# Performance work log

Measured on AMD Instinct MI355X. Metric: run time of the kernel, lower is better.

Reference implementation:

```python
import jax, jax.numpy as jnp
import numpy as np

IN_FEATS, N_HIDDEN, N_CLASSES = 128, 256, 32
N0, N1, B = 614400, 40960, 4096
F0, F1 = 15, 10
BN_EPS = 1e-5


def setup_inputs() -> dict:
    key = jax.random.key(0)
    ks = jax.random.split(key, 20)
    s = 0.02
    inp = {
        "x": jax.random.uniform(ks[0], (N0, IN_FEATS), jnp.float32) * 10.0,
        "nbr0": jax.random.randint(ks[1], (N1, F0), 0, N0, jnp.int32),
        "nbr1": jax.random.randint(ks[2], (B, F1), 0, N1, jnp.int32),
        # layer0: SAGEConv(128->256, 'pool')
        "W_pool": jax.random.normal(ks[3], (IN_FEATS, IN_FEATS), jnp.float32) * s,
        "b_pool": jnp.zeros((IN_FEATS,), jnp.float32),
        "W_self0": jax.random.normal(ks[4], (N_HIDDEN, IN_FEATS), jnp.float32) * s,
        "W_neigh0": jax.random.normal(ks[5], (N_HIDDEN, IN_FEATS), jnp.float32) * s,
        "b0": jnp.zeros((N_HIDDEN,), jnp.float32),
        # BatchNorm1d(n_hidden)
        "gamma0": jnp.ones((N_HIDDEN,), jnp.float32),
        "beta0": jnp.zeros((N_HIDDEN,), jnp.float32),
        # layer1: SAGEConv(256->32, 'lstm'); torch LSTM gate order i,f,g,o
        "W_ih": jax.random.normal(ks[6], (4 * N_HIDDEN, N_HIDDEN), jnp.float32) * s,
        "W_hh": jax.random.normal(ks[7], (4 * N_HIDDEN, N_HIDDEN), jnp.float32) * s,
        "b_ih": jnp.zeros((4 * N_HIDDEN,), jnp.float32),
        "b_hh": jnp.zeros((4 * N_HIDDEN,), jnp.float32),
        "W_self1": jax.random.normal(ks[8], (N_CLASSES, N_HIDDEN), jnp.float32) * s,
        "W_neigh1": jax.random.normal(ks[9], (N_CLASSES, N_HIDDEN), jnp.float32) * s,
        "b1": jnp.zeros((N_CLASSES,), jnp.float32),
    }
    return inp


def _lstm_agg(seq, W_ih, W_hh, b_ih, b_hh):
    # seq: [B, K, H]; run LSTM over K neighbor steps, return final hidden [B, H]
    Bsz, _, H = seq.shape
    xs = jnp.swapaxes(seq, 0, 1)  # [K, B, H]

    def step(carry, x_t):
        h_t, c_t = carry
        g = x_t @ W_ih.T + b_ih + h_t @ W_hh.T + b_hh  # [B, 4H]
        i, f, gg, o = jnp.split(g, 4, axis=-1)
        c = jax.nn.sigmoid(f) * c_t + jax.nn.sigmoid(i) * jnp.tanh(gg)
        h = jax.nn.sigmoid(o) * jnp.tanh(c)
        return (h, c), None

    init = (jnp.zeros((Bsz, H), seq.dtype), jnp.zeros((Bsz, H), seq.dtype))
    (hT, _), _ = jax.lax.scan(step, init, xs)
    return hT


def reference(x, nbr0, nbr1, W_pool, b_pool, W_self0, W_neigh0, b0,
              gamma0, beta0, W_ih, W_hh, b_ih, b_hh, W_self1, W_neigh1, b1):
    n1 = nbr0.shape[0]
    b = nbr1.shape[0]
    h = jnp.log(x + 1.0)  # [N0, in_feats]

    # --- layer 0: SAGEConv 'pool' ---
    hp = jax.nn.relu(h @ W_pool.T + b_pool)           # [N0, in_feats]
    h_neigh = jnp.max(hp[nbr0], axis=1)               # [N1, in_feats]
    h0 = h[:n1] @ W_self0.T + h_neigh @ W_neigh0.T + b0  # [N1, n_hidden]

    # BN (training stats) + relu (dropout p=0)
    mu = jnp.mean(h0, axis=0)
    var = jnp.var(h0, axis=0)
    h0 = (h0 - mu) * jax.lax.rsqrt(var + BN_EPS) * gamma0 + beta0
    h0 = jax.nn.relu(h0)

    # --- layer 1: SAGEConv 'lstm' ---
    seq = h0[nbr1]                                    # [B, F1, n_hidden]
    h_neigh1 = _lstm_agg(seq, W_ih, W_hh, b_ih, b_hh)  # [B, n_hidden]
    out = h0[:b] @ W_self1.T + h_neigh1 @ W_neigh1.T + b1  # [B, n_classes]
    return out
```

## Files before the change

kernel.cpp:

```cpp
#include <hip/hip_runtime.h>

#define N0v 614400
#define N1v 40960
#define BATCHv 4096

typedef __attribute__((ext_vector_type(8))) short short8;
typedef __attribute__((ext_vector_type(4))) float floatx4;

static __device__ __forceinline__ float flog1p(float v) { return __logf(v + 1.0f); }
static __device__ __forceinline__ float sigf(float v) { return 1.0f / (1.0f + __expf(-v)); }
static __device__ __forceinline__ float tanhfast(float v) {
    return 1.0f - 2.0f / (__expf(2.0f * v) + 1.0f);
}
static __device__ __forceinline__ unsigned short f2bf(float f) {
    union { float f; unsigned u; } v; v.f = f;
    unsigned r = v.u + 0x7FFFu + ((v.u >> 16) & 1u);
    return (unsigned short)(r >> 16);
}
static __device__ __forceinline__ float bf2f(unsigned short u) {
    return __uint_as_float(((unsigned)u) << 16);
}

__global__ __launch_bounds__(256) void cvt_weights_kernel(
    const float* __restrict__ Wp, const float* __restrict__ Ws0,
    const float* __restrict__ Wn0, const float* __restrict__ Wih,
    const float* __restrict__ Whh, const float* __restrict__ bih,
    const float* __restrict__ bhh,
    unsigned short* __restrict__ Wpb, unsigned short* __restrict__ Ws0b,
    unsigned short* __restrict__ Wn0b, unsigned short* __restrict__ Wihb,
    unsigned short* __restrict__ Whhb, float* __restrict__ bsum)
{
    const int g = blockIdx.x * 256 + threadIdx.x;
    if (g < 16384)            Wpb[g] = f2bf(Wp[g]);
    else if (g < 49152)       Ws0b[g - 16384] = f2bf(Ws0[g - 16384]);
    else if (g < 81920)       Wn0b[g - 49152] = f2bf(Wn0[g - 49152]);
    else if (g < 344064)      Wihb[g - 81920] = f2bf(Wih[g - 81920]);
    else if (g < 606208)      Whhb[g - 344064] = f2bf(Whh[g - 344064]);
    else if (g < 607232) { const int i = g - 606208; bsum[i] = bih[i] + bhh[i]; }
}

__global__ __launch_bounds__(256) void pool_max_kernel(
    const float* __restrict__ x, const int* __restrict__ nbr0,
    const unsigned short* __restrict__ Wpb, const float* __restrict__ bp,
    unsigned short* __restrict__ hnb)
{
    __shared__ unsigned short smem[64 * 72 + 128 * 72];
    __shared__ unsigned red[512];
    __shared__ int nodes[64];
    unsigned short* aT = smem;
    unsigned short* wT = smem + 64 * 72;

    const int tid = threadIdx.x;
    const size_t base = (size_t)blockIdx.x * 60;
    if (tid < 64) nodes[tid] = (tid < 60) ? nbr0[base + tid] : 0;
    for (int i = tid; i < 512; i += 256) red[i] = 0u;

    const int lane = tid & 63, wv = tid >> 6;
    const int ml = lane & 15, q = lane >> 4, qk = q * 8;

    floatx4 acc[8];
#pragma unroll
    for (int ct = 0; ct < 8; ++ct) acc[ct] = (floatx4){0.f, 0.f, 0.f, 0.f};

    for (int kc = 0; kc < 2; ++kc) {
        __syncthreads();
        for (int i = tid; i < 512; i += 256) {
            const int row = i >> 3, seg = i & 7;
            short8 o = {0, 0, 0, 0, 0, 0, 0, 0};
            if (row < 60) {
                const float* s = x + (size_t)nodes[row] * 128 + kc * 64 + seg * 8;
                const float4 f0 = *(const float4*)s;
                const float4 f1 = *(const float4*)(s + 4);
                o[0] = (short)f2bf(flog1p(f0.x)); o[1] = (short)f2bf(flog1p(f0.y));
                o[2] = (short)f2bf(flog1p(f0.z)); o[3] = (short)f2bf(flog1p(f0.w));
                o[4] = (short)f2bf(flog1p(f1.x)); o[5] = (short)f2bf(flog1p(f1.y));
                o[6] = (short)f2bf(flog1p(f1.z)); o[7] = (short)f2bf(flog1p(f1.w));
            }
            *(short8*)&aT[row * 72 + seg * 8] = o;
        }
        for (int i = tid; i < 1024; i += 256) {
            const int row = i >> 3, seg = i & 7;
            *(short8*)&wT[row * 72 + seg * 8] =
                *(const short8*)&Wpb[(size_t)row * 128 + kc * 64 + seg * 8];
        }
        __syncthreads();
#pragma unroll
        for (int k0 = 0; k0 < 64; k0 += 32) {
            const short8 a = *(const short8*)&aT[(wv * 16 + ml) * 72 + k0 + qk];
#pragma unroll
            for (int ct = 0; ct < 8; ++ct) {
                const short8 b = *(const short8*)&wT[(ct * 16 + ml) * 72 + k0 + qk];
                acc[ct] = __builtin_amdgcn_mfma_f32_16x16x32_bf16(a, b, acc[ct], 0, 0, 0);
            }
        }
    }
    __syncthreads();
#pragma unroll
    for (int ct = 0; ct < 8; ++ct) {
        const int col = ct * 16 + ml;
        const float bb = bp[col];
#pragma unroll
        for (int r = 0; r < 4; ++r) {
            const int row = wv * 16 + q * 4 + r;
            if (row < 60) {
                const float v = fmaxf(acc[ct][r] + bb, 0.0f);
                atomicMax(&red[(row / 15) * 128 + col], __float_as_uint(v));
            }
        }
    }
    __syncthreads();
    for (int i = tid; i < 512; i += 256)
        hnb[(size_t)blockIdx.x * 512 + i] = f2bf(__uint_as_float(red[i]));
}

__global__ __launch_bounds__(256) void h0_kernel(
    const float* __restrict__ x, const unsigned short* __restrict__ hnb,
    const unsigned short* __restrict__ Ws0b, const unsigned short* __restrict__ Wn0b,
    const float* __restrict__ b0, unsigned short* __restrict__ h0bf,
    float* __restrict__ bn_sum, float* __restrict__ bn_sq)
{
    __shared__ unsigned short smem[64 * 72 + 128 * 72];
    unsigned short* aT = smem;
    unsigned short* wT = smem + 64 * 72;

    const int tid = threadIdx.x;
    const int m0 = blockIdx.x * 64, c0 = blockIdx.y * 128;
    const int lane = tid & 63, wv = tid >> 6;
    const int ml = lane & 15, q = lane >> 4, qk = q * 8;

    floatx4 acc[8];
#pragma unroll
    for (int ct = 0; ct < 8; ++ct) acc[ct] = (floatx4){0.f, 0.f, 0.f, 0.f};

    for (int kc = 0; kc < 4; ++kc) {
        __syncthreads();
        for (int i = tid; i < 512; i += 256) {
            const int row = i >> 3, seg = i & 7;
            const int k = kc * 64 + seg * 8;
            if (kc < 2) {
                const float* s = x + (size_t)(m0 + row) * 128 + k;
                const float4 f0 = *(const float4*)s;
                const float4 f1 = *(const float4*)(s + 4);
                short8 o;
                o[0] = (short)f2bf(flog1p(f0.x)); o[1] = (short)f2bf(flog1p(f0.y));
                o[2] = (short)f2bf(flog1p(f0.z)); o[3] = (short)f2bf(flog1p(f0.w));
                o[4] = (short)f2bf(flog1p(f1.x)); o[5] = (short)f2bf(flog1p(f1.y));
                o[6] = (short)f2bf(flog1p(f1.z)); o[7] = (short)f2bf(flog1p(f1.w));
                *(short8*)&aT[row * 72 + seg * 8] = o;
            } else {
                *(short8*)&aT[row * 72 + seg * 8] =
                    *(const short8*)&hnb[(size_t)(m0 + row) * 128 + (k - 128)];
            }
        }
        for (int i = tid; i < 1024; i += 256) {
            const int row = i >> 3, seg = i & 7;
            const int k = kc * 64 + seg * 8;
            const size_t cg = (size_t)(c0 + row);
            *(short8*)&wT[row * 72 + seg * 8] = (kc < 2)
                ? *(const short8*)&Ws0b[cg * 128 + k]
                : *(const short8*)&Wn0b[cg * 128 + (k - 128)];
        }
        __syncthreads();
#pragma unroll
        for (int k0 = 0; k0 < 64; k0 += 32) {
            const short8 a = *(const short8*)&aT[(wv * 16 + ml) * 72 + k0 + qk];
#pragma unroll
            for (int ct = 0; ct < 8; ++ct) {
                const short8 b = *(const short8*)&wT[(ct * 16 + ml) * 72 + k0 + qk];
                acc[ct] = __builtin_amdgcn_mfma_f32_16x16x32_bf16(a, b, acc[ct], 0, 0, 0);
            }
        }
    }
    __syncthreads();
    float* scr = (float*)smem;
#pragma unroll
    for (int ct = 0; ct < 8; ++ct) {
        const int col = ct * 16 + ml, cg = c0 + col;
        const float bb = b0[cg];
        float s = 0.f, sq = 0.f;
#pragma unroll
        for (int r = 0; r < 4; ++r) {
            const int row = wv * 16 + q * 4 + r;
            const float v = acc[ct][r] + bb;
            h0bf[(size_t)(m0 + row) * 256 + cg] = f2bf(v);
            s += v; sq += v * v;
        }
        scr[(wv * 4 + q) * 128 + col] = s;
        scr[2048 + (wv * 4 + q) * 128 + col] = sq;
    }
    __syncthreads();
    if (tid < 128) {
        float s = 0.f, sq = 0.f;
#pragma unroll
        for (int j = 0; j < 16; ++j) {
            s += scr[j * 128 + tid];
            sq += scr[2048 + j * 128 + tid];
        }
        atomicAdd(&bn_sum[c0 + tid], s);
        atomicAdd(&bn_sq[c0 + tid], sq);
    }
}

__global__ void bn_stats_kernel(const float* __restrict__ bn_sum, const float* __restrict__ bn_sq,
                                const float* __restrict__ gamma, const float* __restrict__ beta,
                                float* __restrict__ scale, float* __restrict__ shift)
{
    const int c = threadIdx.x;
    const float inv_n = 1.0f / (float)N1v;
    const float mu = bn_sum[c] * inv_n;
    const float var = bn_sq[c] * inv_n - mu * mu;
    const float rs = rsqrtf(var + 1e-5f);
    const float sc = rs * gamma[c];
    scale[c] = sc;
    shift[c] = beta[c] - mu * sc;
}

__global__ __launch_bounds__(256) void bn_apply_kernel(
    const unsigned short* __restrict__ h0bf, const float* __restrict__ scale,
    const float* __restrict__ shift, unsigned short* __restrict__ h0nbf)
{
    const int gid = blockIdx.x * 256 + threadIdx.x;
    const int c0 = (gid * 8) & 255;
    const short8 v = *(const short8*)&h0bf[(size_t)gid * 8];
    short8 o;
#pragma unroll
    for (int j = 0; j < 8; ++j) {
        const float f = bf2f((unsigned short)v[j]);
        o[j] = (short)f2bf(fmaxf(fmaf(f, scale[c0 + j], shift[c0 + j]), 0.0f));
    }
    *(short8*)&h0nbf[(size_t)gid * 8] = o;
}

__global__ __launch_bounds__(256) void lstm_step_kernel(
    const unsigned short* __restrict__ h0nbf, const int* __restrict__ nbr1,
    const unsigned short* __restrict__ hbprev, const unsigned short* __restrict__ Wihb,
    const unsigned short* __restrict__ Whhb, const float* __restrict__ bsum,
    float* __restrict__ cst, unsigned short* __restrict__ hb, int t)
{
    __shared__ unsigned short smem[64 * 72 + 128 * 72];
    __shared__ int nodes[64];
    unsigned short* aT = smem;
    unsigned short* wT = smem + 64 * 72;

    const int tid = threadIdx.x;
    const int m0 = blockIdx.x * 64, c0h = blockIdx.y * 32;
    const int lane = tid & 63, wv = tid >> 6;
    const int ml = lane & 15, q = lane >> 4, qk = q * 8;

    if (tid < 64) nodes[tid] = nbr1[(size_t)(m0 + tid) * 10 + t];

    floatx4 acc[8];
#pragma unroll
    for (int ct = 0; ct < 8; ++ct) acc[ct] = (floatx4){0.f, 0.f, 0.f, 0.f};

    const int kcN = (t == 0) ? 4 : 8;
    for (int kc = 0; kc < kcN; ++kc) {
        __syncthreads();
        for (int i = tid; i < 512; i += 256) {
            const int row = i >> 3, seg = i & 7;
            const int k = kc * 64 + seg * 8;
            *(short8*)&aT[row * 72 + seg * 8] = (kc < 4)
                ? *(const short8*)&h0nbf[(size_t)nodes[row] * 256 + k]
                : *(const short8*)&hbprev[(size_t)(m0 + row) * 256 + (k - 256)];
        }
        for (int i = tid; i < 1024; i += 256) {
            const int row = i >> 3, seg = i & 7;
            const int k = kc * 64 + seg * 8;
            const size_t wr = (size_t)((row >> 5) * 256 + c0h + (row & 31));
            *(short8*)&wT[row * 72 + seg * 8] = (kc < 4)
                ? *(const short8*)&Wihb[wr * 256 + k]
                : *(const short8*)&Whhb[wr * 256 + (k - 256)];
        }
        __syncthreads();
#pragma unroll
        for (int k0 = 0; k0 < 64; k0 += 32) {
            const short8 a = *(const short8*)&aT[(wv * 16 + ml) * 72 + k0 + qk];
#pragma unroll
            for (int ct = 0; ct < 8; ++ct) {
                const short8 b = *(const short8*)&wT[(ct * 16 + ml) * 72 + k0 + qk];
                acc[ct] = __builtin_amdgcn_mfma_f32_16x16x32_bf16(a, b, acc[ct], 0, 0, 0);
            }
        }
    }
#pragma unroll
    for (int hg = 0; hg < 2; ++hg) {
        const int hcol = hg * 16 + ml;
        const float bi = bsum[c0h + hcol];
        const float bf_ = bsum[256 + c0h + hcol];
        const float bg = bsum[512 + c0h + hcol];
        const float bo = bsum[768 + c0h + hcol];
#pragma unroll
        for (int r = 0; r < 4; ++r) {
            const int row = wv * 16 + q * 4 + r;
            const size_t idx = (size_t)(m0 + row) * 256 + c0h + hcol;
            const float gi = acc[hg][r] + bi;
            const float gf = acc[2 + hg][r] + bf_;
            const float gg = acc[4 + hg][r] + bg;
            const float go = acc[6 + hg][r] + bo;
            float c = sigf(gi) * tanhfast(gg);
            if (t > 0) c += sigf(gf) * cst[idx];
            cst[idx] = c;
            hb[idx] = f2bf(sigf(go) * tanhfast(c));
        }
    }
}

__global__ __launch_bounds__(256) void out_kernel(
    const unsigned short* __restrict__ h0nbf, const unsigned short* __restrict__ hTb,
    const float* __restrict__ Ws1, const float* __restrict__ Wn1,
    const float* __restrict__ b1, float* __restrict__ out)
{
    const int gid = blockIdx.x * 256 + threadIdx.x;
    const int row = gid >> 5, c = gid & 31;
    const unsigned short* a0 = h0nbf + (size_t)row * 256;
    const unsigned short* a1 = hTb + (size_t)row * 256;
    const float* w0 = Ws1 + (size_t)c * 256;
    const float* w1 = Wn1 + (size_t)c * 256;
    float s = b1[c];
#pragma unroll 4
    for (int k8 = 0; k8 < 32; ++k8) {
        const short8 av = *(const short8*)&a0[k8 * 8];
        const short8 bv = *(const short8*)&a1[k8 * 8];
        const float4 wa0 = *(const float4*)&w0[k8 * 8];
        const float4 wa1 = *(const float4*)&w0[k8 * 8 + 4];
        const float4 wb0 = *(const float4*)&w1[k8 * 8];
        const float4 wb1 = *(const float4*)&w1[k8 * 8 + 4];
        s += bf2f((unsigned short)av[0]) * wa0.x + bf2f((unsigned short)av[1]) * wa0.y;
        s += bf2f((unsigned short)av[2]) * wa0.z + bf2f((unsigned short)av[3]) * wa0.w;
        s += bf2f((unsigned short)av[4]) * wa1.x + bf2f((unsigned short)av[5]) * wa1.y;
        s += bf2f((unsigned short)av[6]) * wa1.z + bf2f((unsigned short)av[7]) * wa1.w;
        s += bf2f((unsigned short)bv[0]) * wb0.x + bf2f((unsigned short)bv[1]) * wb0.y;
        s += bf2f((unsigned short)bv[2]) * wb0.z + bf2f((unsigned short)bv[3]) * wb0.w;
        s += bf2f((unsigned short)bv[4]) * wb1.x + bf2f((unsigned short)bv[5]) * wb1.y;
        s += bf2f((unsigned short)bv[6]) * wb1.z + bf2f((unsigned short)bv[7]) * wb1.w;
    }
    out[gid] = s;
}

extern "C" void kernel_launch(void* const* d_in, const int* in_sizes, int n_in,
                              void* d_out, int out_size, void* d_ws, size_t ws_size,
                              hipStream_t stream)
{
    const float* x        = (const float*)d_in[0];
    const int*   nbr0     = (const int*)d_in[1];
    const int*   nbr1     = (const int*)d_in[2];
    const float* W_pool   = (const float*)d_in[3];
    const float* b_pool   = (const float*)d_in[4];
    const float* W_self0  = (const float*)d_in[5];
    const float* W_neigh0 = (const float*)d_in[6];
    const float* b0       = (const float*)d_in[7];
    const float* gamma0   = (const float*)d_in[8];
    const float* beta0    = (const float*)d_in[9];
    const float* W_ih     = (const float*)d_in[10];
    const float* W_hh     = (const float*)d_in[11];
    const float* b_ih     = (const float*)d_in[12];
    const float* b_hh     = (const float*)d_in[13];
    const float* W_self1  = (const float*)d_in[14];
    const float* W_neigh1 = (const float*)d_in[15];
    const float* b1       = (const float*)d_in[16];
    float* out = (float*)d_out;

    char* ws = (char*)d_ws;
    unsigned short* h0bf  = (unsigned short*)(ws);
    unsigned short* hnb   = (unsigned short*)(ws + 20971520);
    unsigned short* h0nbf = (unsigned short*)(ws + 31457280);
    float*          cst   = (float*)(ws + 52428800);
    unsigned short* hb0   = (unsigned short*)(ws + 56623104);
    unsigned short* hb1   = (unsigned short*)(ws + 58720256);
    unsigned short* Wpb   = (unsigned short*)(ws + 60817408);
    unsigned short* Ws0b  = (unsigned short*)(ws + 60850176);
    unsigned short* Wn0b  = (unsigned short*)(ws + 60915712);
    unsigned short* Wihb  = (unsigned short*)(ws + 60981248);
    unsigned short* Whhb  = (unsigned short*)(ws + 61505536);
    float*          bsum  = (float*)(ws + 62029824);
    float*          bn_sum   = (float*)(ws + 62033920);
    float*          bn_sq    = (float*)(ws + 62034944);
    float*          bn_scale = (float*)(ws + 62035968);
    float*          bn_shift = (float*)(ws + 62036992);

    hipMemsetAsync(bn_sum, 0, 2048, stream);

    cvt_weights_kernel<<<2372, 256, 0, stream>>>(W_pool, W_self0, W_neigh0, W_ih, W_hh,
                                                 b_ih, b_hh, Wpb, Ws0b, Wn0b, Wihb, Whhb, bsum);
    pool_max_kernel<<<N1v / 4, 256, 0, stream>>>(x, nbr0, Wpb, b_pool, hnb);
    h0_kernel<<<dim3(N1v / 64, 2), 256, 0, stream>>>(x, hnb, Ws0b, Wn0b, b0,
                                                     h0bf, bn_sum, bn_sq);
    bn_stats_kernel<<<1, 256, 0, stream>>>(bn_sum, bn_sq, gamma0, beta0, bn_scale, bn_shift);
    bn_apply_kernel<<<(N1v * 256 / 8) / 256, 256, 0, stream>>>(h0bf, bn_scale, bn_shift, h0nbf);

    for (int t = 0; t < 10; ++t) {
        const unsigned short* hp = (t & 1) ? hb1 : hb0;
        unsigned short*       hn = (t & 1) ? hb0 : hb1;
        lstm_step_kernel<<<dim3(BATCHv / 64, 8), 256, 0, stream>>>(
            h0nbf, nbr1, hp, Wihb, Whhb, bsum, cst, hn, t);
    }
    out_kernel<<<(BATCHv * 32) / 256, 256, 0, stream>>>(h0nbf, hb0, W_self1, W_neigh1, b1, out);
}
```

Measured before the change: 777.1 us.

## Fuse BN apply, LSTM recurrence and output projection into one persistent kernel

Replaces the BN-apply kernel, the ten per-step LSTM launches and the output kernel with one kernel. Each 512-thread block owns 32 batch rows and keeps h in LDS and c in registers across all steps. BN plus ReLU is applied on the fly to the gathered neighbor rows, and weight fragments are streamed straight from global/L2 with register double-buffering instead of LDS staging. This removes launch overhead, the BN-apply pass and the h/c round trips through global memory. In exchange only 128 blocks are launched, each re-reading the full 1 MB bf16 weight set every step, which may leave the GPU underoccupied.

Result: slower. 885.3 us (+13.9%).

```diff
diff --git a/kernel.cpp b/kernel.cpp
--- a/kernel.cpp
+++ b/kernel.cpp
@@ -215,126 +215,159 @@
     shift[c] = beta[c] - mu * sc;
 }
 
-__global__ __launch_bounds__(256) void bn_apply_kernel(
-    const unsigned short* __restrict__ h0bf, const float* __restrict__ scale,
-    const float* __restrict__ shift, unsigned short* __restrict__ h0nbf)
-{
-    const int gid = blockIdx.x * 256 + threadIdx.x;
-    const int c0 = (gid * 8) & 255;
-    const short8 v = *(const short8*)&h0bf[(size_t)gid * 8];
-    short8 o;
-#pragma unroll
-    for (int j = 0; j < 8; ++j) {
-        const float f = bf2f((unsigned short)v[j]);
-        o[j] = (short)f2bf(fmaxf(fmaf(f, scale[c0 + j], shift[c0 + j]), 0.0f));
-    }
-    *(short8*)&h0nbf[(size_t)gid * 8] = o;
-}
-
-__global__ __launch_bounds__(256) void lstm_step_kernel(
-    const unsigned short* __restrict__ h0nbf, const int* __restrict__ nbr1,
-    const unsigned short* __restrict__ hbprev, const unsigned short* __restrict__ Wihb,
-    const unsigned short* __restrict__ Whhb, const float* __restrict__ bsum,
-    float* __restrict__ cst, unsigned short* __restrict__ hb, int t)
-{
-    __shared__ unsigned short smem[64 * 72 + 128 * 72];
-    __shared__ int nodes[64];
-    unsigned short* aT = smem;
-    unsigned short* wT = smem + 64 * 72;
+__global__ __launch_bounds__(512, 2) void lstm_persist_kernel(
+    const unsigned short* __restrict__ h0bf, const int* __restrict__ nbr1,
+    const unsigned short* __restrict__ Wihb, const unsigned short* __restrict__ Whhb,
+    const float* __restrict__ bsum, const float* __restrict__ bn_scale,
+    const float* __restrict__ bn_shift, const float* __restrict__ Ws1,
+    const float* __restrict__ Wn1, const float* __restrict__ b1,
+    float* __restrict__ out)
+{
+    __shared__ unsigned short aT[32 * 520];
+    __shared__ float sc[256], sh[256];
+    __shared__ int nodes[32];
 
     const int tid = threadIdx.x;
-    const int m0 = blockIdx.x * 64, c0h = blockIdx.y * 32;
+    const int m0 = blockIdx.x * 32;
     const int lane = tid & 63, wv = tid >> 6;
     const int ml = lane & 15, q = lane >> 4, qk = q * 8;
 
-    if (tid < 64) nodes[tid] = nbr1[(size_t)(m0 + tid) * 10 + t];
-
-    floatx4 acc[8];
-#pragma unroll
-    for (int ct = 0; ct < 8; ++ct) acc[ct] = (floatx4){0.f, 0.f, 0.f, 0.f};
-
-    const int kcN = (t == 0) ? 4 : 8;
-    for (int kc = 0; kc < kcN; ++kc) {
-        __syncthreads();
-        for (int i = tid; i < 512; i += 256) {
-            const int row = i >> 3, seg = i & 7;
-            const int k = kc * 64 + seg * 8;
-            *(short8*)&aT[row * 72 + seg * 8] = (kc < 4)
-                ? *(const short8*)&h0nbf[(size_t)nodes[row] * 256 + k]
-                : *(const short8*)&hbprev[(size_t)(m0 + row) * 256 + (k - 256)];
-        }
-        for (int i = tid; i < 1024; i += 256) {
-            const int row = i >> 3, seg = i & 7;
-            const int k = kc * 64 + seg * 8;
-            const size_t wr = (size_t)((row >> 5) * 256 + c0h + (row & 31));
-            *(short8*)&wT[row * 72 + seg * 8] = (kc < 4)
-                ? *(const short8*)&Wihb[wr * 256 + k]
-                : *(const short8*)&Whhb[wr * 256 + (k - 256)];
-        }
-        __syncthreads();
-#pragma unroll
-        for (int k0 = 0; k0 < 64; k0 += 32) {
-            const short8 a = *(const short8*)&aT[(wv * 16 + ml) * 72 + k0 + qk];
+    if (tid < 256) { sc[tid] = bn_scale[tid]; sh[tid] = bn_shift[tid]; }
+
+    int wroff[8];
+#pragma unroll
+    for (int ct = 0; ct < 8; ++ct)
+        wroff[ct] = ((ct >> 1) * 256 + wv * 32 + (ct & 1) * 16 + ml) * 256;
+
+    float bias[4][2];
+#pragma unroll
+    for (int g = 0; g < 4; ++g)
+#pragma unroll
+        for (int hg = 0; hg < 2; ++hg)
+            bias[g][hg] = bsum[g * 256 + wv * 32 + hg * 16 + ml];
+
+    float cs[2][2][4];
+#pragma unroll
+    for (int rt = 0; rt < 2; ++rt)
+#pragma unroll
+        for (int hg = 0; hg < 2; ++hg)
+#pragma unroll
+            for (int r = 0; r < 4; ++r) cs[rt][hg][r] = 0.f;
+
+    for (int t = 0; t < 10; ++t) {
+        if (tid < 32) nodes[tid] = nbr1[(size_t)(m0 + tid) * 10 + t];
+        __syncthreads();
+        for (int i = tid; i < 1024; i += 512) {
+            const int row = i >> 5, seg = i & 31;
+            const short8 v = *(const short8*)&h0bf[(size_t)nodes[row] * 256 + seg * 8];
+            short8 o;
+#pragma unroll
+            for (int j = 0; j < 8; ++j) {
+                const float f = fmaxf(fmaf(bf2f((unsigned short)v[j]),
+                                           sc[seg * 8 + j], sh[seg * 8 + j]), 0.0f);
+                o[j] = (short)f2bf(f);
+            }
+            *(short8*)&aT[row * 520 + seg * 8] = o;
+        }
+        __syncthreads();
+
+        floatx4 acc[2][8];
+#pragma unroll
+        for (int rt = 0; rt < 2; ++rt)
+#pragma unroll
+            for (int ct = 0; ct < 8; ++ct) acc[rt][ct] = (floatx4){0.f, 0.f, 0.f, 0.f};
+
+        const int ksN = (t == 0) ? 8 : 16;
+        short8 bcur[8], bnxt[8];
+#pragma unroll
+        for (int ct = 0; ct < 8; ++ct)
+            bcur[ct] = *(const short8*)&Wihb[wroff[ct] + qk];
+        for (int ks = 0; ks < ksN; ++ks) {
+            const int ksn = ks + 1;
+            if (ksn < ksN) {
+                const unsigned short* wb = (ksn < 8) ? Wihb : Whhb;
+                const int koff = (ksn & 7) * 32 + qk;
+#pragma unroll
+                for (int ct = 0; ct < 8; ++ct)
+                    bnxt[ct] = *(const short8*)&wb[wroff[ct] + koff];
+            }
+            const short8 a0 = *(const short8*)&aT[ml * 520 + ks * 32 + qk];
+            const short8 a1 = *(const short8*)&aT[(16 + ml) * 520 + ks * 32 + qk];
 #pragma unroll
             for (int ct = 0; ct < 8; ++ct) {
-                const short8 b = *(const short8*)&wT[(ct * 16 + ml) * 72 + k0 + qk];
-                acc[ct] = __builtin_amdgcn_mfma_f32_16x16x32_bf16(a, b, acc[ct], 0, 0, 0);
-            }
-        }
-    }
-#pragma unroll
-    for (int hg = 0; hg < 2; ++hg) {
-        const int hcol = hg * 16 + ml;
-        const float bi = bsum[c0h + hcol];
-        const float bf_ = bsum[256 + c0h + hcol];
-        const float bg = bsum[512 + c0h + hcol];
-        const float bo = bsum[768 + c0h + hcol];
-#pragma unroll
-        for (int r = 0; r < 4; ++r) {
-            const int row = wv * 16 + q * 4 + r;
-            const size_t idx = (size_t)(m0 + row) * 256 + c0h + hcol;
-            const float gi = acc[hg][r] + bi;
-            const float gf = acc[2 + hg][r] + bf_;
-            const float gg = acc[4 + hg][r] + bg;
-            const float go = acc[6 + hg][r] + bo;
-            float c = sigf(gi) * tanhfast(gg);
-            if (t > 0) c += sigf(gf) * cst[idx];
-            cst[idx] = c;
-            hb[idx] = f2bf(sigf(go) * tanhfast(c));
-        }
-    }
-}
-
-__global__ __launch_bounds__(256) void out_kernel(
-    const unsigned short* __restrict__ h0nbf, const unsigned short* __restrict__ hTb,
-    const float* __restrict__ Ws1, const float* __restrict__ Wn1,
-    const float* __restrict__ b1, float* __restrict__ out)
-{
-    const int gid = blockIdx.x * 256 + threadIdx.x;
-    const int row = gid >> 5, c = gid & 31;
-    const unsigned short* a0 = h0nbf + (size_t)row * 256;
-    const unsigned short* a1 = hTb + (size_t)row * 256;
-    const float* w0 = Ws1 + (size_t)c * 256;
-    const float* w1 = Wn1 + (size_t)c * 256;
-    float s = b1[c];
+                acc[0][ct] = __builtin_amdgcn_mfma_f32_16x16x32_bf16(a0, bcur[ct], acc[0][ct], 0, 0, 0);
+                acc[1][ct] = __builtin_amdgcn_mfma_f32_16x16x32_bf16(a1, bcur[ct], acc[1][ct], 0, 0, 0);
+            }
+#pragma unroll
+            for (int ct = 0; ct < 8; ++ct) bcur[ct] = bnxt[ct];
+        }
+
+        unsigned short hv[2][2][4];
+#pragma unroll
+        for (int rt = 0; rt < 2; ++rt)
+#pragma unroll
+            for (int hg = 0; hg < 2; ++hg)
+#pragma unroll
+                for (int r = 0; r < 4; ++r) {
+                    const float gi = acc[rt][0 + hg][r] + bias[0][hg];
+                    const float gf = acc[rt][2 + hg][r] + bias[1][hg];
+                    const float gg = acc[rt][4 + hg][r] + bias[2][hg];
+                    const float go = acc[rt][6 + hg][r] + bias[3][hg];
+                    float c = sigf(gi) * tanhfast(gg);
+                    if (t > 0) c += sigf(gf) * cs[rt][hg][r];
+                    cs[rt][hg][r] = c;
+                    hv[rt][hg][r] = f2bf(sigf(go) * tanhfast(c));
+                }
+        __syncthreads();
+#pragma unroll
+        for (int rt = 0; rt < 2; ++rt)
+#pragma unroll
+            for (int hg = 0; hg < 2; ++hg)
+#pragma unroll
+                for (int r = 0; r < 4; ++r)
+                    aT[(rt * 16 + q * 4 + r) * 520 + 256 + wv * 32 + hg * 16 + ml] =
+                        hv[rt][hg][r];
+    }
+
+    for (int i = tid; i < 1024; i += 512) {
+        const int row = i >> 5, seg = i & 31;
+        const short8 v = *(const short8*)&h0bf[(size_t)(m0 + row) * 256 + seg * 8];
+        short8 o;
+#pragma unroll
+        for (int j = 0; j < 8; ++j) {
+            const float f = fmaxf(fmaf(bf2f((unsigned short)v[j]),
+                                       sc[seg * 8 + j], sh[seg * 8 + j]), 0.0f);
+            o[j] = (short)f2bf(f);
+        }
+        *(short8*)&aT[row * 520 + seg * 8] = o;
+    }
+    __syncthreads();
+
+    for (int e = tid; e < 1024; e += 512) {
+        const int row = e >> 5, cls = e & 31;
+        const float* w0 = Ws1 + (size_t)cls * 256;
+        const float* w1 = Wn1 + (size_t)cls * 256;
+        const unsigned short* ar = &aT[row * 520];
+        float s = b1[cls];
 #pragma unroll 4
-    for (int k8 = 0; k8 < 32; ++k8) {
-        const short8 av = *(const short8*)&a0[k8 * 8];
-        const short8 bv = *(const short8*)&a1[k8 * 8];
-        const float4 wa0 = *(const float4*)&w0[k8 * 8];
-        const float4 wa1 = *(const float4*)&w0[k8 * 8 + 4];
-        const float4 wb0 = *(const float4*)&w1[k8 * 8];
-        const float4 wb1 = *(const float4*)&w1[k8 * 8 + 4];
-        s += bf2f((unsigned short)av[0]) * wa0.x + bf2f((unsigned short)av[1]) * wa0.y;
-        s += bf2f((unsigned short)av[2]) * wa0.z + bf2f((unsigned short)av[3]) * wa0.w;
-        s += bf2f((unsigned short)av[4]) * wa1.x + bf2f((unsigned short)av[5]) * wa1.y;
-        s += bf2f((unsigned short)av[6]) * wa1.z + bf2f((unsigned short)av[7]) * wa1.w;
-        s += bf2f((unsigned short)bv[0]) * wb0.x + bf2f((unsigned short)bv[1]) * wb0.y;
-        s += bf2f((unsigned short)bv[2]) * wb0.z + bf2f((unsigned short)bv[3]) * wb0.w;
-        s += bf2f((unsigned short)bv[4]) * wb1.x + bf2f((unsigned short)bv[5]) * wb1.y;
-        s += bf2f((unsigned short)bv[6]) * wb1.z + bf2f((unsigned short)bv[7]) * wb1.w;
-    }
-    out[gid] = s;
+        for (int k8 = 0; k8 < 32; ++k8) {
+            const short8 av = *(const short8*)&ar[k8 * 8];
+            const short8 bv = *(const short8*)&ar[256 + k8 * 8];
+            const float4 wa0 = *(const float4*)&w0[k8 * 8];
+            const float4 wa1 = *(const float4*)&w0[k8 * 8 + 4];
+            const float4 wb0 = *(const float4*)&w1[k8 * 8];
+            const float4 wb1 = *(const float4*)&w1[k8 * 8 + 4];
+            s += bf2f((unsigned short)av[0]) * wa0.x + bf2f((unsigned short)av[1]) * wa0.y;
+            s += bf2f((unsigned short)av[2]) * wa0.z + bf2f((unsigned short)av[3]) * wa0.w;
+            s += bf2f((unsigned short)av[4]) * wa1.x + bf2f((unsigned short)av[5]) * wa1.y;
+            s += bf2f((unsigned short)av[6]) * wa1.z + bf2f((unsigned short)av[7]) * wa1.w;
+            s += bf2f((unsigned short)bv[0]) * wb0.x + bf2f((unsigned short)bv[1]) * wb0.y;
+            s += bf2f((unsigned short)bv[2]) * wb0.z + bf2f((unsigned short)bv[3]) * wb0.w;
+            s += bf2f((unsigned short)bv[4]) * wb1.x + bf2f((unsigned short)bv[5]) * wb1.y;
+            s += bf2f((unsigned short)bv[6]) * wb1.z + bf2f((unsigned short)bv[7]) * wb1.w;
+        }
+        out[(size_t)(m0 + row) * 32 + cls] = s;
+    }
 }
 
 extern "C" void kernel_launch(void* const* d_in, const int* in_sizes, int n_in,
@@ -363,10 +396,6 @@
     char* ws = (char*)d_ws;
     unsigned short* h0bf  = (unsigned short*)(ws);
     unsigned short* hnb   = (unsigned short*)(ws + 20971520);
-    unsigned short* h0nbf = (unsigned short*)(ws + 31457280);
-    float*          cst   = (float*)(ws + 52428800);
-    unsigned short* hb0   = (unsigned short*)(ws + 56623104);
-    unsigned short* hb1   = (unsigned short*)(ws + 58720256);
     unsigned short* Wpb   = (unsigned short*)(ws + 60817408);
     unsigned short* Ws0b  = (unsigned short*)(ws + 60850176);
     unsigned short* Wn0b  = (unsigned short*)(ws + 60915712);
@@ -386,13 +415,6 @@
     h0_kernel<<<dim3(N1v / 64, 2), 256, 0, stream>>>(x, hnb, Ws0b, Wn0b, b0,
                                                      h0bf, bn_sum, bn_sq);
     bn_stats_kernel<<<1, 256, 0, stream>>>(bn_sum, bn_sq, gamma0, beta0, bn_scale, bn_shift);
-    bn_apply_kernel<<<(N1v * 256 / 8) / 256, 256, 0, stream>>>(h0bf, bn_scale, bn_shift, h0nbf);
-
-    for (int t = 0; t < 10; ++t) {
-        const unsigned short* hp = (t & 1) ? hb1 : hb0;
-        unsigned short*       hn = (t & 1) ? hb0 : hb1;
-        lstm_step_kernel<<<dim3(BATCHv / 64, 8), 256, 0, stream>>>(
-            h0nbf, nbr1, hp, Wihb, Whhb, bsum, cst, hn, t);
-    }
-    out_kernel<<<(BATCHv * 32) / 256, 256, 0, stream>>>(h0nbf, hb0, W_self1, W_neigh1, b1, out);
-}
+    lstm_persist_kernel<<<BATCHv / 32, 512, 0, stream>>>(
+        h0bf, nbr1, Wihb, Whhb, bsum, bn_scale, bn_shift, W_self1, W_neigh1, b1, out);
+}
```

## Fuse BatchNorm apply into LSTM gather and output; double pool tile rows

Applied to the files above, without the earlier changes.

Removes the separate bn_apply pass over the full 40960x256 hidden matrix. The scale, shift and ReLU are now applied on the fly where rows are gathered, in the LSTM step kernel and in a reworked output kernel that stages its rows in shared memory. The pool-max kernel now handles 120 neighbor rows per block with two row tiles per wave, so each block loads the pool weights once for twice the work. The trade-off is that the BN transform is recomputed on every gather over 10 LSTM steps, and the pool kernel uses more LDS and registers, which may lower occupancy.

Result: slower. 797.4 us (+2.6%).

```diff
diff --git a/kernel.cpp b/kernel.cpp
--- a/kernel.cpp
+++ b/kernel.cpp
@@ -44,30 +44,32 @@
     const unsigned short* __restrict__ Wpb, const float* __restrict__ bp,
     unsigned short* __restrict__ hnb)
 {
-    __shared__ unsigned short smem[64 * 72 + 128 * 72];
-    __shared__ unsigned red[512];
-    __shared__ int nodes[64];
+    __shared__ unsigned short smem[128 * 72 + 128 * 72];
+    __shared__ unsigned red[1024];
+    __shared__ int nodes[128];
     unsigned short* aT = smem;
-    unsigned short* wT = smem + 64 * 72;
+    unsigned short* wT = smem + 128 * 72;
 
     const int tid = threadIdx.x;
-    const size_t base = (size_t)blockIdx.x * 60;
-    if (tid < 64) nodes[tid] = (tid < 60) ? nbr0[base + tid] : 0;
-    for (int i = tid; i < 512; i += 256) red[i] = 0u;
+    const size_t base = (size_t)blockIdx.x * 120;
+    if (tid < 128) nodes[tid] = (tid < 120) ? nbr0[base + tid] : 0;
+    for (int i = tid; i < 1024; i += 256) red[i] = 0u;
 
     const int lane = tid & 63, wv = tid >> 6;
     const int ml = lane & 15, q = lane >> 4, qk = q * 8;
 
-    floatx4 acc[8];
-#pragma unroll
-    for (int ct = 0; ct < 8; ++ct) acc[ct] = (floatx4){0.f, 0.f, 0.f, 0.f};
+    floatx4 acc[2][8];
+#pragma unroll
+    for (int rt = 0; rt < 2; ++rt)
+#pragma unroll
+        for (int ct = 0; ct < 8; ++ct) acc[rt][ct] = (floatx4){0.f, 0.f, 0.f, 0.f};
 
     for (int kc = 0; kc < 2; ++kc) {
         __syncthreads();
-        for (int i = tid; i < 512; i += 256) {
+        for (int i = tid; i < 1024; i += 256) {
             const int row = i >> 3, seg = i & 7;
             short8 o = {0, 0, 0, 0, 0, 0, 0, 0};
-            if (row < 60) {
+            if (row < 120) {
                 const float* s = x + (size_t)nodes[row] * 128 + kc * 64 + seg * 8;
                 const float4 f0 = *(const float4*)s;
                 const float4 f1 = *(const float4*)(s + 4);
@@ -86,31 +88,36 @@
         __syncthreads();
 #pragma unroll
         for (int k0 = 0; k0 < 64; k0 += 32) {
-            const short8 a = *(const short8*)&aT[(wv * 16 + ml) * 72 + k0 + qk];
-#pragma unroll
-            for (int ct = 0; ct < 8; ++ct) {
-                const short8 b = *(const short8*)&wT[(ct * 16 + ml) * 72 + k0 + qk];
-                acc[ct] = __builtin_amdgcn_mfma_f32_16x16x32_bf16(a, b, acc[ct], 0, 0, 0);
-            }
-        }
-    }
-    __syncthreads();
-#pragma unroll
-    for (int ct = 0; ct < 8; ++ct) {
-        const int col = ct * 16 + ml;
-        const float bb = bp[col];
-#pragma unroll
-        for (int r = 0; r < 4; ++r) {
-            const int row = wv * 16 + q * 4 + r;
-            if (row < 60) {
-                const float v = fmaxf(acc[ct][r] + bb, 0.0f);
-                atomicMax(&red[(row / 15) * 128 + col], __float_as_uint(v));
-            }
-        }
-    }
-    __syncthreads();
-    for (int i = tid; i < 512; i += 256)
-        hnb[(size_t)blockIdx.x * 512 + i] = f2bf(__uint_as_float(red[i]));
+#pragma unroll
+            for (int rt = 0; rt < 2; ++rt) {
+                const short8 a = *(const short8*)&aT[((rt * 4 + wv) * 16 + ml) * 72 + k0 + qk];
+#pragma unroll
+                for (int ct = 0; ct < 8; ++ct) {
+                    const short8 b = *(const short8*)&wT[(ct * 16 + ml) * 72 + k0 + qk];
+                    acc[rt][ct] = __builtin_amdgcn_mfma_f32_16x16x32_bf16(a, b, acc[rt][ct], 0, 0, 0);
+                }
+            }
+        }
+    }
+    __syncthreads();
+#pragma unroll
+    for (int rt = 0; rt < 2; ++rt)
+#pragma unroll
+        for (int ct = 0; ct < 8; ++ct) {
+            const int col = ct * 16 + ml;
+            const float bb = bp[col];
+#pragma unroll
+            for (int r = 0; r < 4; ++r) {
+                const int row = (rt * 4 + wv) * 16 + q * 4 + r;
+                if (row < 120) {
+                    const float v = fmaxf(acc[rt][ct][r] + bb, 0.0f);
+                    atomicMax(&red[(row / 15) * 128 + col], __float_as_uint(v));
+                }
+            }
+        }
+    __syncthreads();
+    for (int i = tid; i < 1024; i += 256)
+        hnb[(size_t)blockIdx.x * 1024 + i] = f2bf(__uint_as_float(red[i]));
 }
 
 __global__ __launch_bounds__(256) void h0_kernel(
@@ -215,29 +222,15 @@
     shift[c] = beta[c] - mu * sc;
 }
 
-__global__ __launch_bounds__(256) void bn_apply_kernel(
-    const unsigned short* __restrict__ h0bf, const float* __restrict__ scale,
-    const float* __restrict__ shift, unsigned short* __restrict__ h0nbf)
-{
-    const int gid = blockIdx.x * 256 + threadIdx.x;
-    const int c0 = (gid * 8) & 255;
-    const short8 v = *(const short8*)&h0bf[(size_t)gid * 8];
-    short8 o;
-#pragma unroll
-    for (int j = 0; j < 8; ++j) {
-        const float f = bf2f((unsigned short)v[j]);
-        o[j] = (short)f2bf(fmaxf(fmaf(f, scale[c0 + j], shift[c0 + j]), 0.0f));
-    }
-    *(short8*)&h0nbf[(size_t)gid * 8] = o;
-}
-
 __global__ __launch_bounds__(256) void lstm_step_kernel(
-    const unsigned short* __restrict__ h0nbf, const int* __restrict__ nbr1,
+    const unsigned short* __restrict__ h0bf, const int* __restrict__ nbr1,
     const unsigned short* __restrict__ hbprev, const unsigned short* __restrict__ Wihb,
     const unsigned short* __restrict__ Whhb, const float* __restrict__ bsum,
+    const float* __restrict__ bn_scale, const float* __restrict__ bn_shift,
     float* __restrict__ cst, unsigned short* __restrict__ hb, int t)
 {
     __shared__ unsigned short smem[64 * 72 + 128 * 72];
+    __shared__ float scl[256], shl[256];
     __shared__ int nodes[64];
     unsigned short* aT = smem;
     unsigned short* wT = smem + 64 * 72;
@@ -248,6 +241,8 @@
     const int ml = lane & 15, q = lane >> 4, qk = q * 8;
 
     if (tid < 64) nodes[tid] = nbr1[(size_t)(m0 + tid) * 10 + t];
+    scl[tid] = bn_scale[tid];
+    shl[tid] = bn_shift[tid];
 
     floatx4 acc[8];
 #pragma unroll
@@ -259,9 +254,20 @@
         for (int i = tid; i < 512; i += 256) {
             const int row = i >> 3, seg = i & 7;
             const int k = kc * 64 + seg * 8;
-            *(short8*)&aT[row * 72 + seg * 8] = (kc < 4)
-                ? *(const short8*)&h0nbf[(size_t)nodes[row] * 256 + k]
-                : *(const short8*)&hbprev[(size_t)(m0 + row) * 256 + (k - 256)];
+            if (kc < 4) {
+                const short8 v = *(const short8*)&h0bf[(size_t)nodes[row] * 256 + k];
+                short8 o;
+#pragma unroll
+                for (int j = 0; j < 8; ++j) {
+                    const float f = fmaxf(fmaf(bf2f((unsigned short)v[j]),
+                                               scl[k + j], shl[k + j]), 0.0f);
+                    o[j] = (short)f2bf(f);
+                }
+                *(short8*)&aT[row * 72 + seg * 8] = o;
+            } else {
+                *(short8*)&aT[row * 72 + seg * 8] =
+                    *(const short8*)&hbprev[(size_t)(m0 + row) * 256 + (k - 256)];
+            }
         }
         for (int i = tid; i < 1024; i += 256) {
             const int row = i >> 3, seg = i & 7;
@@ -306,17 +312,47 @@
 }
 
 __global__ __launch_bounds__(256) void out_kernel(
-    const unsigned short* __restrict__ h0nbf, const unsigned short* __restrict__ hTb,
+    const unsigned short* __restrict__ h0bf, const unsigned short* __restrict__ hTb,
+    const float* __restrict__ bn_scale, const float* __restrict__ bn_shift,
     const float* __restrict__ Ws1, const float* __restrict__ Wn1,
     const float* __restrict__ b1, float* __restrict__ out)
 {
-    const int gid = blockIdx.x * 256 + threadIdx.x;
-    const int row = gid >> 5, c = gid & 31;
-    const unsigned short* a0 = h0nbf + (size_t)row * 256;
-    const unsigned short* a1 = hTb + (size_t)row * 256;
-    const float* w0 = Ws1 + (size_t)c * 256;
-    const float* w1 = Wn1 + (size_t)c * 256;
-    float s = b1[c];
+    __shared__ unsigned short aS[8 * 256];
+    __shared__ unsigned short hS[8 * 256];
+    __shared__ float scl[256], shl[256];
+
+    const int tid = threadIdx.x;
+    const int m0 = blockIdx.x * 8;
+    scl[tid] = bn_scale[tid];
+    shl[tid] = bn_shift[tid];
+    __syncthreads();
+
+    for (int i = tid; i < 512; i += 256) {
+        const int sel = i >> 8, idx = i & 255;
+        const int row = idx >> 5, seg = idx & 31;
+        if (sel == 0) {
+            const short8 v = *(const short8*)&h0bf[(size_t)(m0 + row) * 256 + seg * 8];
+            short8 o;
+#pragma unroll
+            for (int j = 0; j < 8; ++j) {
+                const float f = fmaxf(fmaf(bf2f((unsigned short)v[j]),
+                                           scl[seg * 8 + j], shl[seg * 8 + j]), 0.0f);
+                o[j] = (short)f2bf(f);
+            }
+            *(short8*)&aS[row * 256 + seg * 8] = o;
+        } else {
+            *(short8*)&hS[row * 256 + seg * 8] =
+                *(const short8*)&hTb[(size_t)(m0 + row) * 256 + seg * 8];
+        }
+    }
+    __syncthreads();
+
+    const int row = tid >> 5, cls = tid & 31;
+    const float* w0 = Ws1 + (size_t)cls * 256;
+    const float* w1 = Wn1 + (size_t)cls * 256;
+    const unsigned short* a0 = &aS[row * 256];
+    const unsigned short* a1 = &hS[row * 256];
+    float s = b1[cls];
 #pragma unroll 4
     for (int k8 = 0; k8 < 32; ++k8) {
         const short8 av = *(const short8*)&a0[k8 * 8];
@@ -334,7 +370,7 @@
         s += bf2f((unsigned short)bv[4]) * wb1.x + bf2f((unsigned short)bv[5]) * wb1.y;
         s += bf2f((unsigned short)bv[6]) * wb1.z + bf2f((unsigned short)bv[7]) * wb1.w;
     }
-    out[gid] = s;
+    out[(size_t)(m0 + row) * 32 + cls] = s;
 }
 
 extern "C" void kernel_launch(void* const* d_in, const int* in_sizes, int n_in,
@@ -363,7 +399,6 @@
     char* ws = (char*)d_ws;
     unsigned short* h0bf  = (unsigned short*)(ws);
     unsigned short* hnb   = (unsigned short*)(ws + 20971520);
-    unsigned short* h0nbf = (unsigned short*)(ws + 31457280);
     float*          cst   = (float*)(ws + 52428800);
     unsigned short* hb0   = (unsigned short*)(ws + 56623104);
     unsigned short* hb1   = (unsigned short*)(ws + 58720256);
@@ -382,17 +417,17 @@
 
     cvt_weights_kernel<<<2372, 256, 0, stream>>>(W_pool, W_self0, W_neigh0, W_ih, W_hh,
                                                  b_ih, b_hh, Wpb, Ws0b, Wn0b, Wihb, Whhb, bsum);
-    pool_max_kernel<<<N1v / 4, 256, 0, stream>>>(x, nbr0, Wpb, b_pool, hnb);
+    pool_max_kernel<<<N1v / 8, 256, 0, stream>>>(x, nbr0, Wpb, b_pool, hnb);
     h0_kernel<<<dim3(N1v / 64, 2), 256, 0, stream>>>(x, hnb, Ws0b, Wn0b, b0,
                                                      h0bf, bn_sum, bn_sq);
     bn_stats_kernel<<<1, 256, 0, stream>>>(bn_sum, bn_sq, gamma0, beta0, bn_scale, bn_shift);
-    bn_apply_kernel<<<(N1v * 256 / 8) / 256, 256, 0, stream>>>(h0bf, bn_scale, bn_shift, h0nbf);
 
     for (int t = 0; t < 10; ++t) {
         const unsigned short* hp = (t & 1) ? hb1 : hb0;
         unsigned short*       hn = (t & 1) ? hb0 : hb1;
         lstm_step_kernel<<<dim3(BATCHv / 64, 8), 256, 0, stream>>>(
-            h0nbf, nbr1, hp, Wihb, Whhb, bsum, cst, hn, t);
-    }
-    out_kernel<<<(BATCHv * 32) / 256, 256, 0, stream>>>(h0nbf, hb0, W_self1, W_neigh1, b1, out);
-}
+            h0bf, nbr1, hp, Wihb, Whhb, bsum, bn_scale, bn_shift, cst, hn, t);
+    }
+    out_kernel<<<BATCHv / 8, 256, 0, stream>>>(h0bf, hb0, bn_scale, bn_shift,
+                                               W_self1, W_neigh1, b1, out);
+}
```

## Load MFMA operands directly from global memory, drop LDS staging and barriers

Applied to the files above, without the earlier changes.

The pool_max, h0 and LSTM step kernels no longer stage activation and weight tiles through shared memory with __syncthreads. Each lane now loads its MFMA A and B fragments straight from global memory, leaning on L1/L2 to serve the weights that all waves share. The output kernel now stages its 8 input rows in LDS so the 32 class threads of a row share them. This removes the LDS round trip and block barriers, but multiplies redundant global and cache traffic for the weight fragments, and the narrow 16-byte per-lane row loads coalesce poorly.

Measured after the change: 998.6 us. +28.5%, slower.

```diff
diff --git a/kernel.cpp b/kernel.cpp
--- a/kernel.cpp
+++ b/kernel.cpp
@@ -44,54 +44,37 @@
     const unsigned short* __restrict__ Wpb, const float* __restrict__ bp,
     unsigned short* __restrict__ hnb)
 {
-    __shared__ unsigned short smem[64 * 72 + 128 * 72];
     __shared__ unsigned red[512];
-    __shared__ int nodes[64];
-    unsigned short* aT = smem;
-    unsigned short* wT = smem + 64 * 72;
 
     const int tid = threadIdx.x;
     const size_t base = (size_t)blockIdx.x * 60;
-    if (tid < 64) nodes[tid] = (tid < 60) ? nbr0[base + tid] : 0;
-    for (int i = tid; i < 512; i += 256) red[i] = 0u;
-
     const int lane = tid & 63, wv = tid >> 6;
     const int ml = lane & 15, q = lane >> 4, qk = q * 8;
 
+    for (int i = tid; i < 512; i += 256) red[i] = 0u;
+
+    const int row16 = wv * 16 + ml;
+    const int arow = (row16 < 60) ? row16 : 0;
+    const int node = nbr0[base + arow];
+    const float* xr = x + (size_t)node * 128;
+
     floatx4 acc[8];
 #pragma unroll
     for (int ct = 0; ct < 8; ++ct) acc[ct] = (floatx4){0.f, 0.f, 0.f, 0.f};
 
-    for (int kc = 0; kc < 2; ++kc) {
-        __syncthreads();
-        for (int i = tid; i < 512; i += 256) {
-            const int row = i >> 3, seg = i & 7;
-            short8 o = {0, 0, 0, 0, 0, 0, 0, 0};
-            if (row < 60) {
-                const float* s = x + (size_t)nodes[row] * 128 + kc * 64 + seg * 8;
-                const float4 f0 = *(const float4*)s;
-                const float4 f1 = *(const float4*)(s + 4);
-                o[0] = (short)f2bf(flog1p(f0.x)); o[1] = (short)f2bf(flog1p(f0.y));
-                o[2] = (short)f2bf(flog1p(f0.z)); o[3] = (short)f2bf(flog1p(f0.w));
-                o[4] = (short)f2bf(flog1p(f1.x)); o[5] = (short)f2bf(flog1p(f1.y));
-                o[6] = (short)f2bf(flog1p(f1.z)); o[7] = (short)f2bf(flog1p(f1.w));
-            }
-            *(short8*)&aT[row * 72 + seg * 8] = o;
-        }
-        for (int i = tid; i < 1024; i += 256) {
-            const int row = i >> 3, seg = i & 7;
-            *(short8*)&wT[row * 72 + seg * 8] =
-                *(const short8*)&Wpb[(size_t)row * 128 + kc * 64 + seg * 8];
-        }
-        __syncthreads();
-#pragma unroll
-        for (int k0 = 0; k0 < 64; k0 += 32) {
-            const short8 a = *(const short8*)&aT[(wv * 16 + ml) * 72 + k0 + qk];
-#pragma unroll
-            for (int ct = 0; ct < 8; ++ct) {
-                const short8 b = *(const short8*)&wT[(ct * 16 + ml) * 72 + k0 + qk];
-                acc[ct] = __builtin_amdgcn_mfma_f32_16x16x32_bf16(a, b, acc[ct], 0, 0, 0);
-            }
+#pragma unroll
+    for (int ks = 0; ks < 4; ++ks) {
+        const float4 f0 = *(const float4*)&xr[ks * 32 + qk];
+        const float4 f1 = *(const float4*)&xr[ks * 32 + qk + 4];
+        short8 a;
+        a[0] = (short)f2bf(flog1p(f0.x)); a[1] = (short)f2bf(flog1p(f0.y));
+        a[2] = (short)f2bf(flog1p(f0.z)); a[3] = (short)f2bf(flog1p(f0.w));
+        a[4] = (short)f2bf(flog1p(f1.x)); a[5] = (short)f2bf(flog1p(f1.y));
+        a[6] = (short)f2bf(flog1p(f1.z)); a[7] = (short)f2bf(flog1p(f1.w));
+#pragma unroll
+        for (int ct = 0; ct < 8; ++ct) {
+            const short8 b = *(const short8*)&Wpb[(size_t)(ct * 16 + ml) * 128 + ks * 32 + qk];
+            acc[ct] = __builtin_amdgcn_mfma_f32_16x16x32_bf16(a, b, acc[ct], 0, 0, 0);
         }
     }
     __syncthreads();
@@ -119,60 +102,46 @@
     const float* __restrict__ b0, unsigned short* __restrict__ h0bf,
     float* __restrict__ bn_sum, float* __restrict__ bn_sq)
 {
-    __shared__ unsigned short smem[64 * 72 + 128 * 72];
-    unsigned short* aT = smem;
-    unsigned short* wT = smem + 64 * 72;
+    __shared__ float scr[4096];
 
     const int tid = threadIdx.x;
     const int m0 = blockIdx.x * 64, c0 = blockIdx.y * 128;
     const int lane = tid & 63, wv = tid >> 6;
     const int ml = lane & 15, q = lane >> 4, qk = q * 8;
 
+    const int arow = m0 + wv * 16 + ml;
+    const float* xr = x + (size_t)arow * 128;
+    const unsigned short* hr = hnb + (size_t)arow * 128;
+
     floatx4 acc[8];
 #pragma unroll
     for (int ct = 0; ct < 8; ++ct) acc[ct] = (floatx4){0.f, 0.f, 0.f, 0.f};
 
-    for (int kc = 0; kc < 4; ++kc) {
-        __syncthreads();
-        for (int i = tid; i < 512; i += 256) {
-            const int row = i >> 3, seg = i & 7;
-            const int k = kc * 64 + seg * 8;
-            if (kc < 2) {
-                const float* s = x + (size_t)(m0 + row) * 128 + k;
-                const float4 f0 = *(const float4*)s;
-                const float4 f1 = *(const float4*)(s + 4);
-                short8 o;
-                o[0] = (short)f2bf(flog1p(f0.x)); o[1] = (short)f2bf(flog1p(f0.y));
-                o[2] = (short)f2bf(flog1p(f0.z)); o[3] = (short)f2bf(flog1p(f0.w));
-                o[4] = (short)f2bf(flog1p(f1.x)); o[5] = (short)f2bf(flog1p(f1.y));
-                o[6] = (short)f2bf(flog1p(f1.z)); o[7] = (short)f2bf(flog1p(f1.w));
-                *(short8*)&aT[row * 72 + seg * 8] = o;
-            } else {
-                *(short8*)&aT[row * 72 + seg * 8] =
-                    *(const short8*)&hnb[(size_t)(m0 + row) * 128 + (k - 128)];
-            }
-        }
-        for (int i = tid; i < 1024; i += 256) {
-            const int row = i >> 3, seg = i & 7;
-            const int k = kc * 64 + seg * 8;
-            const size_t cg = (size_t)(c0 + row);
-            *(short8*)&wT[row * 72 + seg * 8] = (kc < 2)
-                ? *(const short8*)&Ws0b[cg * 128 + k]
-                : *(const short8*)&Wn0b[cg * 128 + (k - 128)];
-        }
-        __syncthreads();
-#pragma unroll
-        for (int k0 = 0; k0 < 64; k0 += 32) {
-            const short8 a = *(const short8*)&aT[(wv * 16 + ml) * 72 + k0 + qk];
-#pragma unroll
-            for (int ct = 0; ct < 8; ++ct) {
-                const short8 b = *(const short8*)&wT[(ct * 16 + ml) * 72 + k0 + qk];
-                acc[ct] = __builtin_amdgcn_mfma_f32_16x16x32_bf16(a, b, acc[ct], 0, 0, 0);
-            }
-        }
-    }
-    __syncthreads();
-    float* scr = (float*)smem;
+#pragma unroll
+    for (int ks = 0; ks < 4; ++ks) {
+        const float4 f0 = *(const float4*)&xr[ks * 32 + qk];
+        const float4 f1 = *(const float4*)&xr[ks * 32 + qk + 4];
+        short8 a;
+        a[0] = (short)f2bf(flog1p(f0.x)); a[1] = (short)f2bf(flog1p(f0.y));
+        a[2] = (short)f2bf(flog1p(f0.z)); a[3] = (short)f2bf(flog1p(f0.w));
+        a[4] = (short)f2bf(flog1p(f1.x)); a[5] = (short)f2bf(flog1p(f1.y));
+        a[6] = (short)f2bf(flog1p(f1.z)); a[7] = (short)f2bf(flog1p(f1.w));
+#pragma unroll
+        for (int ct = 0; ct < 8; ++ct) {
+            const short8 b = *(const short8*)&Ws0b[(size_t)(c0 + ct * 16 + ml) * 128 + ks * 32 + qk];
+            acc[ct] = __builtin_amdgcn_mfma_f32_16x16x32_bf16(a, b, acc[ct], 0, 0, 0);
+        }
+    }
+#pragma unroll
+    for (int ks = 0; ks < 4; ++ks) {
+        const short8 a = *(const short8*)&hr[ks * 32 + qk];
+#pragma unroll
+        for (int ct = 0; ct < 8; ++ct) {
+            const short8 b = *(const short8*)&Wn0b[(size_t)(c0 + ct * 16 + ml) * 128 + ks * 32 + qk];
+            acc[ct] = __builtin_amdgcn_mfma_f32_16x16x32_bf16(a, b, acc[ct], 0, 0, 0);
+        }
+    }
+
 #pragma unroll
     for (int ct = 0; ct < 8; ++ct) {
         const int col = ct * 16 + ml, cg = c0 + col;
@@ -237,51 +206,46 @@
     const unsigned short* __restrict__ Whhb, const float* __restrict__ bsum,
     float* __restrict__ cst, unsigned short* __restrict__ hb, int t)
 {
-    __shared__ unsigned short smem[64 * 72 + 128 * 72];
-    __shared__ int nodes[64];
-    unsigned short* aT = smem;
-    unsigned short* wT = smem + 64 * 72;
-
     const int tid = threadIdx.x;
     const int m0 = blockIdx.x * 64, c0h = blockIdx.y * 32;
     const int lane = tid & 63, wv = tid >> 6;
     const int ml = lane & 15, q = lane >> 4, qk = q * 8;
 
-    if (tid < 64) nodes[tid] = nbr1[(size_t)(m0 + tid) * 10 + t];
+    const int arow = m0 + wv * 16 + ml;
+    const int node = nbr1[(size_t)arow * 10 + t];
+    const unsigned short* ag = h0nbf + (size_t)node * 256;
+    const unsigned short* ah = hbprev + (size_t)arow * 256;
+
+    size_t wroff[8];
+#pragma unroll
+    for (int ct = 0; ct < 8; ++ct)
+        wroff[ct] = (size_t)((ct >> 1) * 256 + c0h + (ct & 1) * 16 + ml) * 256;
 
     floatx4 acc[8];
 #pragma unroll
     for (int ct = 0; ct < 8; ++ct) acc[ct] = (floatx4){0.f, 0.f, 0.f, 0.f};
 
-    const int kcN = (t == 0) ? 4 : 8;
-    for (int kc = 0; kc < kcN; ++kc) {
-        __syncthreads();
-        for (int i = tid; i < 512; i += 256) {
-            const int row = i >> 3, seg = i & 7;
-            const int k = kc * 64 + seg * 8;
-            *(short8*)&aT[row * 72 + seg * 8] = (kc < 4)
-                ? *(const short8*)&h0nbf[(size_t)nodes[row] * 256 + k]
-                : *(const short8*)&hbprev[(size_t)(m0 + row) * 256 + (k - 256)];
-        }
-        for (int i = tid; i < 1024; i += 256) {
-            const int row = i >> 3, seg = i & 7;
-            const int k = kc * 64 + seg * 8;
-            const size_t wr = (size_t)((row >> 5) * 256 + c0h + (row & 31));
-            *(short8*)&wT[row * 72 + seg * 8] = (kc < 4)
-                ? *(const short8*)&Wihb[wr * 256 + k]
-                : *(const short8*)&Whhb[wr * 256 + (k - 256)];
-        }
-        __syncthreads();
-#pragma unroll
-        for (int k0 = 0; k0 < 64; k0 += 32) {
-            const short8 a = *(const short8*)&aT[(wv * 16 + ml) * 72 + k0 + qk];
+#pragma unroll
+    for (int ks = 0; ks < 8; ++ks) {
+        const short8 a = *(const short8*)&ag[ks * 32 + qk];
+#pragma unroll
+        for (int ct = 0; ct < 8; ++ct) {
+            const short8 b = *(const short8*)&Wihb[wroff[ct] + ks * 32 + qk];
+            acc[ct] = __builtin_amdgcn_mfma_f32_16x16x32_bf16(a, b, acc[ct], 0, 0, 0);
+        }
+    }
+    if (t > 0) {
+#pragma unroll
+        for (int ks = 0; ks < 8; ++ks) {
+            const short8 a = *(const short8*)&ah[ks * 32 + qk];
 #pragma unroll
             for (int ct = 0; ct < 8; ++ct) {
-                const short8 b = *(const short8*)&wT[(ct * 16 + ml) * 72 + k0 + qk];
+                const short8 b = *(const short8*)&Whhb[wroff[ct] + ks * 32 + qk];
                 acc[ct] = __builtin_amdgcn_mfma_f32_16x16x32_bf16(a, b, acc[ct], 0, 0, 0);
             }
         }
     }
+
 #pragma unroll
     for (int hg = 0; hg < 2; ++hg) {
         const int hcol = hg * 16 + ml;
@@ -293,7 +257,7 @@
         for (int r = 0; r < 4; ++r) {
             const int row = wv * 16 + q * 4 + r;
             const size_t idx = (size_t)(m0 + row) * 256 + c0h + hcol;
-            const float gi = acc[hg][r] + bi;
+            const float gi = acc[0 + hg][r] + bi;
             const float gf = acc[2 + hg][r] + bf_;
             const float gg = acc[4 + hg][r] + bg;
             const float go = acc[6 + hg][r] + bo;
@@ -310,13 +274,30 @@
     const float* __restrict__ Ws1, const float* __restrict__ Wn1,
     const float* __restrict__ b1, float* __restrict__ out)
 {
-    const int gid = blockIdx.x * 256 + threadIdx.x;
-    const int row = gid >> 5, c = gid & 31;
-    const unsigned short* a0 = h0nbf + (size_t)row * 256;
-    const unsigned short* a1 = hTb + (size_t)row * 256;
-    const float* w0 = Ws1 + (size_t)c * 256;
-    const float* w1 = Wn1 + (size_t)c * 256;
-    float s = b1[c];
+    __shared__ unsigned short aS[8 * 256];
+    __shared__ unsigned short hS[8 * 256];
+
+    const int tid = threadIdx.x;
+    const int m0 = blockIdx.x * 8;
+
+    for (int i = tid; i < 512; i += 256) {
+        const int sel = i >> 8, idx = i & 255;
+        const int row = idx >> 5, seg = idx & 31;
+        if (sel == 0)
+            *(short8*)&aS[row * 256 + seg * 8] =
+                *(const short8*)&h0nbf[(size_t)(m0 + row) * 256 + seg * 8];
+        else
+            *(short8*)&hS[row * 256 + seg * 8] =
+                *(const short8*)&hTb[(size_t)(m0 + row) * 256 + seg * 8];
+    }
+    __syncthreads();
+
+    const int row = tid >> 5, cls = tid & 31;
+    const float* w0 = Ws1 + (size_t)cls * 256;
+    const float* w1 = Wn1 + (size_t)cls * 256;
+    const unsigned short* a0 = &aS[row * 256];
+    const unsigned short* a1 = &hS[row * 256];
+    float s = b1[cls];
 #pragma unroll 4
     for (int k8 = 0; k8 < 32; ++k8) {
         const short8 av = *(const short8*)&a0[k8 * 8];
@@ -334,7 +315,7 @@
         s += bf2f((unsigned short)bv[4]) * wb1.x + bf2f((unsigned short)bv[5]) * wb1.y;
         s += bf2f((unsigned short)bv[6]) * wb1.z + bf2f((unsigned short)bv[7]) * wb1.w;
     }
-    out[gid] = s;
+    out[(size_t)(m0 + row) * 32 + cls] = s;
 }
 
 extern "C" void kernel_launch(void* const* d_in, const int* in_sizes, int n_in,
@@ -394,5 +375,5 @@
         lstm_step_kernel<<<dim3(BATCHv / 64, 8), 256, 0, stream>>>(
             h0nbf, nbr1, hp, Wihb, Whhb, bsum, cst, hn, t);
     }
-    out_kernel<<<(BATCHv * 32) / 256, 256, 0, stream>>>(h0nbf, hb0, W_self1, W_neigh1, b1, out);
-}
+    out_kernel<<<BATCHv / 8, 256, 0, stream>>>(h0nbf, hb0, W_self1, W_neigh1, b1, out);
+}
```
